# Performance work log

Hardware: AMD Instinct MI355X
Metric: run time of the kernel (lower is better)

## Reference

```python
import jax, jax.numpy as jnp
import numpy as np

DIM = 1024
EPS = 1e-5


def setup_inputs() -> dict:
    key = jax.random.key(0)
    ks = jax.random.split(key, 7)
    C = DIM
    x = jax.random.normal(ks[0], (4, 4096, C), dtype=jnp.float32)
    norm_w = jnp.ones((C,), dtype=jnp.float32)
    norm_b = jnp.zeros((C,), dtype=jnp.float32)
    s = 1.0 / np.sqrt(C)
    qkv_w = jax.random.uniform(ks[1], (3 * C, C), dtype=jnp.float32, minval=-s, maxval=s)
    qkv_b = jax.random.uniform(ks[2], (3 * C,), dtype=jnp.float32, minval=-s, maxval=s)
    proj_w = jax.random.uniform(ks[3], (C, C), dtype=jnp.float32, minval=-s, maxval=s)
    proj_b = jax.random.uniform(ks[4], (C,), dtype=jnp.float32, minval=-s, maxval=s)
    return {"x": x, "norm_w": norm_w, "norm_b": norm_b, "qkv_w": qkv_w,
            "qkv_b": qkv_b, "proj_w": proj_w, "proj_b": proj_b}


def _layernorm(x, w, b):
    mu = jnp.mean(x, axis=-1, keepdims=True)
    var = jnp.mean(jnp.square(x - mu), axis=-1, keepdims=True)
    return (x - mu) * jax.lax.rsqrt(var + EPS) * w + b


def reference(x, norm_w, norm_b, qkv_w, qkv_b, proj_w, proj_b):
    B, T, C = x.shape
    residual = x
    h = _layernorm(x, norm_w, norm_b)
    qkv = jnp.einsum('btc,oc->bto', h, qkv_w) + qkv_b  # [B,T,3C]
    q, k, v = qkv[..., :C], qkv[..., C:2 * C], qkv[..., 2 * C:]
    attn = jnp.einsum('btc,bsc->bts', q, k) / jnp.sqrt(jnp.float32(C))  # raw QK^T, no softmax
    o = jnp.einsum('bts,bsc->btc', attn, v)
    o = jnp.einsum('btc,oc->bto', o, proj_w) + proj_b
    return residual + o  # dropout is identity in eval mode
```

## Files before the change

kernel.cpp:

```cpp
#include <hip/hip_runtime.h>

typedef _Float16 f16;
typedef _Float16 f16x4 __attribute__((ext_vector_type(4)));
typedef _Float16 f16x8 __attribute__((ext_vector_type(8)));
typedef float f32x4 __attribute__((ext_vector_type(4)));

#define AS1 __attribute__((address_space(1)))
#define AS3 __attribute__((address_space(3)))

__device__ __forceinline__ void gl_lds16(const f16* g, f16* l) {
  __builtin_amdgcn_global_load_lds((const AS1 void*)g, (AS3 void*)l, 16, 0, 0);
}

__global__ __launch_bounds__(256) void ln_kernel(const float* __restrict__ x,
                                                 const float* __restrict__ gw,
                                                 const float* __restrict__ gb,
                                                 f16* __restrict__ H) {
  const int wv = threadIdx.x >> 6, lane = threadIdx.x & 63;
  const long row = (long)blockIdx.x * 4 + wv;
  const float* xr = x + row * 1024;
  float4 v[4];
  float s = 0.f, s2 = 0.f;
#pragma unroll
  for (int j = 0; j < 4; ++j) {
    v[j] = ((const float4*)xr)[lane + 64 * j];
    s  += v[j].x + v[j].y + v[j].z + v[j].w;
    s2 += v[j].x * v[j].x + v[j].y * v[j].y + v[j].z * v[j].z + v[j].w * v[j].w;
  }
#pragma unroll
  for (int off = 32; off > 0; off >>= 1) {
    s  += __shfl_xor(s, off);
    s2 += __shfl_xor(s2, off);
  }
  const float mu = s * (1.0f / 1024.0f);
  const float rstd = rsqrtf(s2 * (1.0f / 1024.0f) - mu * mu + 1e-5f);
#pragma unroll
  for (int j = 0; j < 4; ++j) {
    const float4 w4 = ((const float4*)gw)[lane + 64 * j];
    const float4 b4 = ((const float4*)gb)[lane + 64 * j];
    f16x4 h;
    h[0] = (f16)((v[j].x - mu) * rstd * w4.x + b4.x);
    h[1] = (f16)((v[j].y - mu) * rstd * w4.y + b4.y);
    h[2] = (f16)((v[j].z - mu) * rstd * w4.z + b4.z);
    h[3] = (f16)((v[j].w - mu) * rstd * w4.w + b4.w);
    *(f16x4*)(H + row * 1024 + (lane + 64 * j) * 4) = h;
  }
}

__global__ __launch_bounds__(256) void transpose_cs_kernel(const f16* __restrict__ H,
                                                           f16* __restrict__ Ht,
                                                           float* __restrict__ hs) {
  __shared__ f16 tile[64][68];
  __shared__ float csum[4][64];
  const int b = blockIdx.z;
  const long Hb  = (long)b * 4096 * 1024;
  const long Htb = (long)b * 1024 * 4096;
  const int t0 = blockIdx.y * 64, c0 = blockIdx.x * 64;
  const int tid = threadIdx.x;
  const int r = tid >> 2, g0 = tid & 3;
#pragma unroll
  for (int i = 0; i < 4; ++i) {
    const int g = g0 + i * 4;
    f16x4 v = *(const f16x4*)(H + Hb + (long)(t0 + r) * 1024 + c0 + g * 4);
    *(f16x4*)&tile[r][g * 4] = v;
  }
  __syncthreads();
  {
    const int cl = tid & 63, rg = tid >> 6;
    float s = 0.f;
#pragma unroll
    for (int rr = 0; rr < 16; ++rr) s += (float)tile[rg * 16 + rr][cl];
    csum[rg][cl] = s;
  }
#pragma unroll
  for (int i = 0; i < 4; ++i) {
    const int g = g0 + i * 4;
    f16x4 v;
    v[0] = tile[g * 4 + 0][r];
    v[1] = tile[g * 4 + 1][r];
    v[2] = tile[g * 4 + 2][r];
    v[3] = tile[g * 4 + 3][r];
    *(f16x4*)(Ht + Htb + (long)(c0 + r) * 4096 + t0 + g * 4) = v;
  }
  __syncthreads();
  if (tid < 64)
    atomicAdd(&hs[b * 1024 + c0 + tid],
              csum[0][tid] + csum[1][tid] + csum[2][tid] + csum[3][tid]);
}

__global__ __launch_bounds__(256) void transcast4(const float* __restrict__ qkv_w,
                                                  const float* __restrict__ proj_w,
                                                  f16* __restrict__ WT3,
                                                  f16* __restrict__ Wh,
                                                  f16* __restrict__ Ph) {
  const int z = blockIdx.z;
  __shared__ f16 tile[64][68];
  const int r0 = blockIdx.y * 64, c0 = blockIdx.x * 64;
  const int tid = threadIdx.x;
  const int r = tid >> 2, g0 = tid & 3;
  if (z == 3) {
#pragma unroll
    for (int i = 0; i < 4; ++i) {
      const int g = g0 + i * 4;
      float4 v = *(const float4*)(proj_w + (long)(r0 + r) * 1024 + c0 + g * 4);
      f16x4 h; h[0]=(f16)v.x; h[1]=(f16)v.y; h[2]=(f16)v.z; h[3]=(f16)v.w;
      *(f16x4*)(Ph + (long)(r0 + r) * 1024 + c0 + g * 4) = h;
    }
    return;
  }
  const float* W = qkv_w + (long)z * 1048576;
  f16* WT = WT3 + (long)z * 1048576;
#pragma unroll
  for (int i = 0; i < 4; ++i) {
    const int g = g0 + i * 4;
    float4 v = *(const float4*)(W + (long)(r0 + r) * 1024 + c0 + g * 4);
    f16x4 h; h[0]=(f16)v.x; h[1]=(f16)v.y; h[2]=(f16)v.z; h[3]=(f16)v.w;
    *(f16x4*)&tile[r][g * 4] = h;
    if (z >= 1)
      *(f16x4*)(Wh + (long)z * 1048576 + (long)(r0 + r) * 1024 + c0 + g * 4) = h;
  }
  __syncthreads();
#pragma unroll
  for (int i = 0; i < 4; ++i) {
    const int g = g0 + i * 4;
    f16x4 v;
    v[0] = tile[g * 4 + 0][r];
    v[1] = tile[g * 4 + 1][r];
    v[2] = tile[g * 4 + 2][r];
    v[3] = tile[g * 4 + 3][r];
    *(f16x4*)(WT + (long)(c0 + r) * 1024 + r0 + g * 4) = v;
  }
}

__device__ __forceinline__ float dot1024(const f16* __restrict__ row,
                                         const float* __restrict__ v) {
  const int lane = threadIdx.x & 63;
  float s = 0.f;
#pragma unroll
  for (int j = 0; j < 2; ++j) {
    const int d = (lane + 64 * j) * 8;
    f16x8 a = *(const f16x8*)(row + d);
    float4 h0 = *(const float4*)(v + d);
    float4 h1 = *(const float4*)(v + d + 4);
    s += (float)a[0] * h0.x + (float)a[1] * h0.y + (float)a[2] * h0.z + (float)a[3] * h0.w
       + (float)a[4] * h1.x + (float)a[5] * h1.y + (float)a[6] * h1.z + (float)a[7] * h1.w;
  }
#pragma unroll
  for (int off = 32; off > 0; off >>= 1) s += __shfl_down(s, off);
  return s;
}

__device__ __forceinline__ float dotf1024(const float* __restrict__ a,
                                          const float* __restrict__ v) {
  const int lane = threadIdx.x & 63;
  float s = 0.f;
#pragma unroll
  for (int j = 0; j < 4; ++j) {
    const int d = (lane + 64 * j) * 4;
    float4 x = *(const float4*)(a + d);
    float4 q = *(const float4*)(v + d);
    s += x.x * q.x + x.y * q.y + x.z * q.z + x.w * q.w;
  }
#pragma unroll
  for (int off = 32; off > 0; off >>= 1) s += __shfl_down(s, off);
  return s;
}

__global__ void gemv3a(const f16* __restrict__ WT3, const f16* __restrict__ Ph,
                       const float* __restrict__ qkv_b, float* __restrict__ ayd,
                       float* __restrict__ scal) {
  if (blockIdx.x == 3072) {
    float s = dotf1024(qkv_b + 1024, qkv_b);
    if ((threadIdx.x & 63) == 0) scal[4] = s;
    return;
  }
  const int which = blockIdx.x >> 10, m = blockIdx.x & 1023;
  const f16* row;
  const float* v;
  if (which == 0)      { row = WT3 + (long)m * 1024;            v = qkv_b + 1024; }
  else if (which == 1) { row = WT3 + 1048576 + (long)m * 1024;  v = qkv_b; }
  else                 { row = Ph + (long)m * 1024;             v = qkv_b + 2048; }
  float s = dot1024(row, v);
  if ((threadIdx.x & 63) == 0) ayd[which * 1024 + m] = s;
}

__global__ void gemv3b(const f16* __restrict__ U, const f16* __restrict__ PWv,
                       const f16* __restrict__ Gh, const float* __restrict__ hs,
                       const float* __restrict__ ayd, float* __restrict__ efz,
                       float* __restrict__ scal) {
  if (blockIdx.x >= 12288) {
    const int b = blockIdx.x - 12288;
    float s = dotf1024(hs + b * 1024, ayd + 1024);
    if ((threadIdx.x & 63) == 0) scal[b] = s;
    return;
  }
  const int sel = blockIdx.x >> 12, r = blockIdx.x & 4095;
  const int b = r >> 10, m = r & 1023;
  const f16* row;
  const float* v;
  if (sel == 0)      { row = U + (long)m * 1024;                       v = hs + b * 1024; }
  else if (sel == 1) { row = PWv + (long)m * 1024;                     v = hs + b * 1024; }
  else               { row = Gh + (long)b * 1048576 + (long)m * 1024;  v = ayd + 1024; }
  float s = dot1024(row, v);
  if ((threadIdx.x & 63) == 0) efz[sel * 4096 + r] = s;
}

__global__ void gemvC2n(const f16* __restrict__ PWv, const float* __restrict__ efz,
                        const float* __restrict__ ayd, const float* __restrict__ scal,
                        const float* __restrict__ proj_b, float* __restrict__ c2) {
  const int b = blockIdx.x >> 10, c = blockIdx.x & 1023;
  float s = dot1024(PWv + (long)c * 1024, efz + 8192 + b * 1024);
  if ((threadIdx.x & 63) == 0) {
    const float d = ayd[2048 + c];
    c2[b * 1024 + c] = (s + d * scal[b] + scal[4] * (efz[4096 + b * 1024 + c] + 4096.f * d))
                         * 0.03125f + proj_b[c];
  }
}

#define GP64_COMMON()                                        \
  const int tid = threadIdx.x;                               \
  const int wave = tid >> 6, lane = tid & 63;                \
  const int lr = lane & 15, lk = lane >> 4;                  \
  const int srow = tid >> 3;                                 \
  const int slc  = (tid & 7) ^ (srow & 7);                   \
  const int kc0 = ((lk) ^ (lr & 7)) * 8;                     \
  const int kc1 = ((4 + lk) ^ (lr & 7)) * 8;

#define GEMM_WAIT8(NBUF_, r_)                                               \
  do {                                                                      \
    if constexpr (NBUF_ == 3) {                                             \
      if ((r_) >= 2)      asm volatile("s_waitcnt vmcnt(16)" ::: "memory"); \
      else if ((r_) == 1) asm volatile("s_waitcnt vmcnt(8)" ::: "memory");  \
      else                asm volatile("s_waitcnt vmcnt(0)" ::: "memory");  \
    } else {                                                                \
      if ((r_) >= 1)      asm volatile("s_waitcnt vmcnt(8)" ::: "memory");  \
      else                asm volatile("s_waitcnt vmcnt(0)" ::: "memory");  \
    }                                                                       \
  } while (0)

#define COMP64_HALF(asb_, bsb_, kc_)                                             \
  do {                                                                           \
    const f16* asb = (asb_);                                                     \
    const f16* bsb = (bsb_);                                                     \
    f16x8 af[4], bf[4];                                                          \
    _Pragma("unroll")                                                            \
    for (int mi = 0; mi < 4; ++mi)                                               \
      af[mi] = *(const f16x8*)(asb + (wm * 64 + mi * 16 + lr) * 64 + (kc_));     \
    _Pragma("unroll")                                                            \
    for (int ni = 0; ni < 4; ++ni)                                               \
      bf[ni] = *(const f16x8*)(bsb + (wn * 64 + ni * 16 + lr) * 64 + (kc_));     \
    _Pragma("unroll")                                                            \
    for (int mi = 0; mi < 4; ++mi)                                               \
      _Pragma("unroll")                                                          \
      for (int ni = 0; ni < 4; ++ni)                                             \
        acc[mi][ni] = __builtin_amdgcn_mfma_f32_16x16x32_f16(af[mi], bf[ni],     \
                                                             acc[mi][ni], 0, 0, 0); \
  } while (0)

#define GEMM_BODY_LOOP(NBUF_, NT_, STAGEM)                       \
  do {                                                           \
    if constexpr (NBUF_ == 3) {                                  \
      STAGEM(0, 0); STAGEM(1, 1);                                \
      int cur = 0, stg = 2;                                      \
      for (int t = 0; t < (NT_); ++t) {                          \
        if (t + 2 < (NT_)) STAGEM(stg, t + 2);                   \
        GEMM_WAIT8(3, (NT_) - 1 - t);                            \
        asm volatile("s_barrier" ::: "memory");                  \
        __builtin_amdgcn_s_setprio(1);                           \
        COMP64_HALF(&As[cur][0], &Bs[cur][0], kc0);              \
        COMP64_HALF(&As[cur][0], &Bs[cur][0], kc1);              \
        __builtin_amdgcn_s_setprio(0);                           \
        asm volatile("s_waitcnt lgkmcnt(0)" ::: "memory");       \
        asm volatile("s_barrier" ::: "memory");                  \
        cur = (cur + 1 == 3) ? 0 : cur + 1;                      \
        stg = (stg + 1 == 3) ? 0 : stg + 1;                      \
      }                                                          \
    } else {                                                     \
      STAGEM(0, 0);                                              \
      int cur = 0;                                               \
      for (int t = 0; t < (NT_); ++t) {                          \
        if (t + 1 < (NT_)) STAGEM(cur ^ 1, t + 1);               \
        GEMM_WAIT8(2, (NT_) - 1 - t);                            \
        asm volatile("s_barrier" ::: "memory");                  \
        __builtin_amdgcn_s_setprio(1);                           \
        COMP64_HALF(&As[cur][0], &Bs[cur][0], kc0);              \
        COMP64_HALF(&As[cur][0], &Bs[cur][0], kc1);              \
        __builtin_amdgcn_s_setprio(0);                           \
        asm volatile("s_waitcnt lgkmcnt(0)" ::: "memory");       \
        asm volatile("s_barrier" ::: "memory");                  \
        cur ^= 1;                                                \
      }                                                          \
    }                                                            \
  } while (0)

template <int MODE>
__global__ __launch_bounds__(256) void gemm128(
    const f16* __restrict__ A, const f16* __restrict__ B, int K,
    long sA, long sB, long sC,
    f16* __restrict__ Ch,
    const float* __restrict__ dvec, const float* __restrict__ evec,
    const float* __restrict__ fvec, const float* __restrict__ avec) {
  const int b = blockIdx.z;
  A += (long)b * sA;
  B += (long)b * sB;
  const int nx = blockIdx.y & 7;
  const int ny = blockIdx.x;

  GP64_COMMON();
  const int wm = wave >> 1, wn = wave & 1;

  __shared__ __align__(16) f16 As[3][8192];
  __shared__ __align__(16) f16 Bs[3][8192];

  const long aoffs = (long)(ny * 128 + srow) * K + slc * 8;
  const long boffs = (long)(nx * 128 + srow) * K + slc * 8;

  f32x4 zero = {0.f, 0.f, 0.f, 0.f};
  f32x4 acc[4][4];
#pragma unroll
  for (int mi = 0; mi < 4; ++mi)
#pragma unroll
    for (int ni = 0; ni < 4; ++ni) acc[mi][ni] = zero;

#define STAGE(buf, kt)                                                              \
  do {                                                                              \
    f16* asb = &As[buf][0];                                                         \
    f16* bsb = &Bs[buf][0];                                                         \
    _Pragma("unroll")                                                               \
    for (int q = 0; q < 4; ++q) {                                                   \
      gl_lds16(A + aoffs + (long)q * 32 * K + (kt) * 64, asb + q * 2048 + tid * 8); \
      gl_lds16(B + boffs + (long)q * 32 * K + (kt) * 64, bsb + q * 2048 + tid * 8); \
    }                                                                               \
  } while (0)

  const int nt = K >> 6;
  GEMM_BODY_LOOP(3, nt, STAGE);
#undef STAGE

  const long cb = (long)b * sC;
  const int m0 = ny * 128 + wm * 64;
  const int n0 = nx * 128 + wn * 64;
#pragma unroll
  for (int mi = 0; mi < 4; ++mi)
#pragma unroll
    for (int ni = 0; ni < 4; ++ni)
#pragma unroll
      for (int j = 0; j < 4; ++j) {
        const int gm = m0 + mi * 16 + lk * 4 + j;
        const int gn = n0 + ni * 16 + lr;
        float val = acc[mi][ni][j];
        if constexpr (MODE == 0) {
          Ch[cb + (long)gm * 1024 + gn] = (f16)val;
        } else {
          const float dm = dvec[gm];
          const float fm = fvec[b * 1024 + gm];
          const float en = evec[b * 1024 + gn];
          const float an = avec[gn];
          val = (val + dm * en + (fm + 4096.f * dm) * an) * 0.03125f;
          Ch[cb + (long)gm * 1024 + gn] = (f16)val;
        }
      }
}

__global__ __launch_bounds__(256) void gemmGUV(const f16* __restrict__ Ht,
                                               const f16* __restrict__ WT3,
                                               const f16* __restrict__ Ph,
                                               f16* __restrict__ part,
                                               f16* __restrict__ U,
                                               f16* __restrict__ PWv) {
  GP64_COMMON();
  const int wm = wave >> 1, wn = wave & 1;

  __shared__ __align__(16) f16 As[2][8192];
  __shared__ __align__(16) f16 Bs[2][8192];

  const int bid = blockIdx.x;
  const f16 *Ab, *Bb;
  long rs;
  int tileid = 0, zz = 0, selt = 0;
  if (bid < 576) {
    zz = bid & 15;
    tileid = bid >> 4;
    const int b = zz & 3, ks4 = zz >> 2;
    int ti = 0, trem = tileid;
    while (trem >= 8 - ti) { trem -= 8 - ti; ++ti; }
    const int tj = ti + trem;
    const f16* Hb = Ht + (long)b * 4194304;
    rs = 4096;
    Ab = Hb + (long)(ti * 128 + srow) * 4096 + (long)ks4 * 1024 + slc * 8;
    Bb = Hb + (long)(tj * 128 + srow) * 4096 + (long)ks4 * 1024 + slc * 8;
  } else {
    const int u = bid - 576;
    selt = (u >> 6) + 1;
    const int t = u & 63;
    const int ny = t >> 3, nxx = t & 7;
    const f16* A0 = (selt == 2) ? Ph : WT3;
    const f16* B0 = (selt == 2) ? (WT3 + 2097152) : (WT3 + 1048576);
    rs = 1024;
    Ab = A0 + (long)(ny * 128 + srow) * 1024 + slc * 8;
    Bb = B0 + (long)(nxx * 128 + srow) * 1024 + slc * 8;
  }

  f32x4 zero = {0.f, 0.f, 0.f, 0.f};
  f32x4 acc[4][4];
#pragma unroll
  for (int mi = 0; mi < 4; ++mi)
#pragma unroll
    for (int ni = 0; ni < 4; ++ni) acc[mi][ni] = zero;

#define SAq(buf, kt, q) gl_lds16(Ab + (long)(q) * 32 * rs + (kt) * 64, &As[buf][(q) * 2048] + tid * 8)
#define SBq(buf, kt, q) gl_lds16(Bb + (long)(q) * 32 * rs + (kt) * 64, &Bs[buf][(q) * 2048] + tid * 8)

  const int nt = 16;
  SBq(0, 0, 0); SBq(0, 0, 1); SBq(0, 0, 2); SBq(0, 0, 3);
  SAq(0, 0, 0); SAq(0, 0, 2); SAq(0, 0, 1); SAq(0, 0, 3);

  int cur = 0;
  for (int t = 0; t < nt; ++t) {
    const f16* asb = &As[cur][0];
    const f16* bsb = &Bs[cur][0];
    const int nb = cur ^ 1;
    const bool st = (t + 1 < nt);
    f16x8 bf[4][2], af[2][2];

    asm volatile("s_waitcnt vmcnt(2)" ::: "memory");
    asm volatile("s_barrier" ::: "memory");
#pragma unroll
    for (int ni = 0; ni < 4; ++ni) {
      bf[ni][0] = *(const f16x8*)(bsb + (wn * 64 + ni * 16 + lr) * 64 + kc0);
      bf[ni][1] = *(const f16x8*)(bsb + (wn * 64 + ni * 16 + lr) * 64 + kc1);
    }
#pragma unroll
    for (int mi = 0; mi < 2; ++mi) {
      af[mi][0] = *(const f16x8*)(asb + (wm * 64 + mi * 16 + lr) * 64 + kc0);
      af[mi][1] = *(const f16x8*)(asb + (wm * 64 + mi * 16 + lr) * 64 + kc1);
    }
    if (st) { SBq(nb, t + 1, 0); SBq(nb, t + 1, 1); SBq(nb, t + 1, 2); SBq(nb, t + 1, 3);
              SAq(nb, t + 1, 0); SAq(nb, t + 1, 2); }
    asm volatile("s_waitcnt lgkmcnt(0)" ::: "memory");
    __builtin_amdgcn_s_setprio(1);
#pragma unroll
    for (int ks = 0; ks < 2; ++ks)
#pragma unroll
      for (int mi = 0; mi < 2; ++mi)
#pragma unroll
        for (int ni = 0; ni < 4; ++ni)
          acc[mi][ni] = __builtin_amdgcn_mfma_f32_16x16x32_f16(af[mi][ks], bf[ni][ks],
                                                               acc[mi][ni], 0, 0, 0);
    __builtin_amdgcn_s_setprio(0);
    asm volatile("s_barrier" ::: "memory");

    if (st) asm volatile("s_waitcnt vmcnt(6)" ::: "memory");
    else    asm volatile("s_waitcnt vmcnt(0)" ::: "memory");
    asm volatile("s_barrier" ::: "memory");
#pragma unroll
    for (int mi = 0; mi < 2; ++mi) {
      af[mi][0] = *(const f16x8*)(asb + (wm * 64 + (mi + 2) * 16 + lr) * 64 + kc0);
      af[mi][1] = *(const f16x8*)(asb + (wm * 64 + (mi + 2) * 16 + lr) * 64 + kc1);
    }
    if (st) { SAq(nb, t + 1, 1); SAq(nb, t + 1, 3); }
    asm volatile("s_waitcnt lgkmcnt(0)" ::: "memory");
    __builtin_amdgcn_s_setprio(1);
#pragma unroll
    for (int ks = 0; ks < 2; ++ks)
#pragma unroll
      for (int mi = 0; mi < 2; ++mi)
#pragma unroll
        for (int ni = 0; ni < 4; ++ni)
          acc[mi + 2][ni] = __builtin_amdgcn_mfma_f32_16x16x32_f16(af[mi][ks], bf[ni][ks],
                                                                   acc[mi + 2][ni], 0, 0, 0);
    __builtin_amdgcn_s_setprio(0);
    asm volatile("s_barrier" ::: "memory");

    cur ^= 1;
  }
#undef SAq
#undef SBq

  if (selt == 0) {
    f16* P = part + ((long)zz * 36 + tileid) * 16384;
#pragma unroll
    for (int mi = 0; mi < 4; ++mi)
#pragma unroll
      for (int ni = 0; ni < 4; ++ni)
#pragma unroll
        for (int j = 0; j < 4; ++j) {
          const int gm = wm * 64 + mi * 16 + lk * 4 + j;
          const int gn = wn * 64 + ni * 16 + lr;
          P[gm * 128 + gn] = (f16)acc[mi][ni][j];
        }
  } else {
    const int u = bid - 576;
    const int t = u & 63;
    const int ny = t >> 3, nxx = t & 7;
    f16* C = (selt == 2) ? PWv : U;
    const int m0 = ny * 128 + wm * 64;
    const int n0 = nxx * 128 + wn * 64;
#pragma unroll
    for (int mi = 0; mi < 4; ++mi)
#pragma unroll
      for (int ni = 0; ni < 4; ++ni)
#pragma unroll
        for (int j = 0; j < 4; ++j) {
          const int gm = m0 + mi * 16 + lk * 4 + j;
          const int gn = n0 + ni * 16 + lr;
          C[(long)gm * 1024 + gn] = (f16)acc[mi][ni][j];
        }
  }
}

__global__ __launch_bounds__(512) void gemm256f(
    const f16* __restrict__ A,
    const f16* __restrict__ Bw,
    const float* __restrict__ resid,
    const float* __restrict__ c2v,
    float* __restrict__ outF) {
  const int lin = blockIdx.y * 4 + blockIdx.x;
  const int xcd = lin & 7, slot = lin >> 3;
  const int ny = xcd * 8 + (slot >> 2);
  const int nx = slot & 3;
  const int bb = ny >> 4;

  GP64_COMMON();
  const int wm = wave >> 2, wn = wave & 3;

  __shared__ __align__(16) f16 As[2][16384];
  __shared__ __align__(16) f16 Bs[2][16384];

  const f16* Ab = A + (long)ny * 262144;
  const f16* Bb = Bw + (long)bb * 1048576 + (long)nx * 262144;
  const long offs = (long)srow * 1024 + slc * 8;

  f32x4 zero = {0.f, 0.f, 0.f, 0.f};
  f32x4 acc[8][4];
#pragma unroll
  for (int mi = 0; mi < 8; ++mi)
#pragma unroll
    for (int ni = 0; ni < 4; ++ni) acc[mi][ni] = zero;

#define SA(buf, kt, q) gl_lds16(Ab + offs + (long)(q) * 65536 + (kt) * 64, &As[buf][(q) * 4096] + tid * 8)
#define SB(buf, kt, q) gl_lds16(Bb + offs + (long)(q) * 65536 + (kt) * 64, &Bs[buf][(q) * 4096] + tid * 8)

#define RD_BF(dst, bsb, kc)                                                       \
  _Pragma("unroll")                                                               \
  for (int ni = 0; ni < 4; ++ni)                                                  \
    dst[ni] = *(const f16x8*)((bsb) + (wn * 64 + ni * 16 + lr) * 64 + (kc));
#define RD_AF(dst, asb, mh, kc)                                                   \
  _Pragma("unroll")                                                               \
  for (int mi = 0; mi < 4; ++mi)                                                  \
    dst[mi] = *(const f16x8*)((asb) + (wm * 128 + (mh) * 64 + mi * 16 + lr) * 64 + (kc));
#define MF16(af_, bf_, mo)                                                        \
  __builtin_amdgcn_s_setprio(1);                                                  \
  _Pragma("unroll")                                                               \
  for (int mi = 0; mi < 4; ++mi)                                                  \
    _Pragma("unroll")                                                             \
    for (int ni = 0; ni < 4; ++ni)                                                \
      acc[(mo) + mi][ni] = __builtin_amdgcn_mfma_f32_16x16x32_f16(af_[mi], bf_[ni], \
                                                                  acc[(mo) + mi][ni], 0, 0, 0); \
  __builtin_amdgcn_s_setprio(0);

  const int nt = 16;
  SB(0, 0, 0); SB(0, 0, 1); SB(0, 0, 2); SB(0, 0, 3);
  SA(0, 0, 0); SA(0, 0, 2); SA(0, 0, 1); SA(0, 0, 3);

  int cur = 0;
  for (int t = 0; t < nt; ++t) {
    const f16* asb = &As[cur][0];
    const f16* bsb = &Bs[cur][0];
    const int nb = cur ^ 1;
    const bool st = (t + 1 < nt);
    f16x8 bf[4], af[4];

    asm volatile("s_waitcnt vmcnt(2)" ::: "memory");
    asm volatile("s_barrier" ::: "memory");
    RD_BF(bf, bsb, kc0);
    RD_AF(af, asb, 0, kc0);
    if (st) { SB(nb, t + 1, 0); SB(nb, t + 1, 1); }
    asm volatile("s_waitcnt lgkmcnt(0)" ::: "memory");
    MF16(af, bf, 0);
    asm volatile("s_barrier" ::: "memory");

    if (st) asm volatile("s_waitcnt vmcnt(2)" ::: "memory");
    else    asm volatile("s_waitcnt vmcnt(0)" ::: "memory");
    asm volatile("s_barrier" ::: "memory");
    RD_AF(af, asb, 1, kc0);
    if (st) { SB(nb, t + 1, 2); SB(nb, t + 1, 3); }
    asm volatile("s_waitcnt lgkmcnt(0)" ::: "memory");
    MF16(af, bf, 4);
    asm volatile("s_barrier" ::: "memory");

    RD_BF(bf, bsb, kc1);
    RD_AF(af, asb, 0, kc1);
    if (st) { SA(nb, t + 1, 0); SA(nb, t + 1, 2); }
    asm volatile("s_waitcnt lgkmcnt(0)" ::: "memory");
    MF16(af, bf, 0);
    asm volatile("s_barrier" ::: "memory");

    RD_AF(af, asb, 1, kc1);
    if (st) { SA(nb, t + 1, 1); SA(nb, t + 1, 3); }
    asm volatile("s_waitcnt lgkmcnt(0)" ::: "memory");
    MF16(af, bf, 4);
    asm volatile("s_barrier" ::: "memory");

    cur ^= 1;
  }
#undef SA
#undef SB
#undef RD_BF
#undef RD_AF
#undef MF16

  asm volatile("s_waitcnt vmcnt(0)" ::: "memory");
  asm volatile("s_barrier" ::: "memory");

  float* weps = ((float*)&As[0][0]) + wave * 1088;
  const int m0 = ny * 256 + wm * 128;
  const int n0 = nx * 256 + wn * 64;
  const int err = lane >> 3;
  const int ecc = (lane & 7) * 4;
  float4 cc2[2];
#pragma unroll
  for (int q = 0; q < 2; ++q)
    cc2[q] = *(const float4*)&c2v[bb * 1024 + n0 + ecc + 32 * q];

#pragma unroll
  for (int mi = 0; mi < 8; ++mi) {
#pragma unroll
    for (int ni = 0; ni < 4; ++ni)
#pragma unroll
      for (int j = 0; j < 4; ++j)
        weps[(lk * 4 + j) * 68 + ni * 16 + lr] = acc[mi][ni][j];
    asm volatile("s_waitcnt lgkmcnt(0)" ::: "memory");
#pragma unroll
    for (int h = 0; h < 2; ++h)
#pragma unroll
      for (int q = 0; q < 2; ++q) {
        const int rr = err + 8 * h;
        const int cc = ecc + 32 * q;
        float4 o = *(const float4*)&weps[rr * 68 + cc];
        const long gbase = (long)(m0 + mi * 16 + rr) * 1024 + n0 + cc;
        const float4 rv = *(const float4*)&resid[gbase];
        float4 ov;
        ov.x = o.x + rv.x + cc2[q].x;
        ov.y = o.y + rv.y + cc2[q].y;
        ov.z = o.z + rv.z + cc2[q].z;
        ov.w = o.w + rv.w + cc2[q].w;
        *(float4*)&outF[gbase] = ov;
      }
  }
}

__global__ __launch_bounds__(256) void treduce(const f16* __restrict__ part,
                                               f16* __restrict__ Gh) {
  const int tileid = blockIdx.x, b = blockIdx.y;
  int ti = 0, trem = tileid;
  while (trem >= 8 - ti) { trem -= 8 - ti; ++ti; }
  const int tj = ti + trem;
  __shared__ f16 tl[128][132];
  const int tid = threadIdx.x;
  f16* Gb = Gh + (long)b * 1048576;
#pragma unroll
  for (int it = 0; it < 16; ++it) {
    const int e = it * 1024 + tid * 4;
    const int r = e >> 7, c = e & 127;
    f16x4 p0 = *(const f16x4*)(part + ((long)(0 * 4 + b) * 36 + tileid) * 16384 + e);
    f16x4 p1 = *(const f16x4*)(part + ((long)(1 * 4 + b) * 36 + tileid) * 16384 + e);
    f16x4 p2 = *(const f16x4*)(part + ((long)(2 * 4 + b) * 36 + tileid) * 16384 + e);
    f16x4 p3 = *(const f16x4*)(part + ((long)(3 * 4 + b) * 36 + tileid) * 16384 + e);
    f16x4 sv;
#pragma unroll
    for (int j = 0; j < 4; ++j)
      sv[j] = (f16)((float)p0[j] + (float)p1[j] + (float)p2[j] + (float)p3[j]);
    *(f16x4*)(Gb + (long)(ti * 128 + r) * 1024 + tj * 128 + c) = sv;
    *(f16x4*)&tl[r][c] = sv;
  }
  if (ti != tj) {
    __syncthreads();
#pragma unroll
    for (int it = 0; it < 16; ++it) {
      const int e = it * 1024 + tid * 4;
      const int r = e >> 7, c = e & 127;
      f16x4 v;
      v[0] = tl[c + 0][r];
      v[1] = tl[c + 1][r];
      v[2] = tl[c + 2][r];
      v[3] = tl[c + 3][r];
      *(f16x4*)(Gb + (long)(tj * 128 + r) * 1024 + ti * 128 + c) = v;
    }
  }
}

extern "C" void kernel_launch(void* const* d_in, const int* in_sizes, int n_in,
                              void* d_out, int out_size, void* d_ws, size_t ws_size,
                              hipStream_t stream) {
  const float* x      = (const float*)d_in[0];
  const float* norm_w = (const float*)d_in[1];
  const float* norm_b = (const float*)d_in[2];
  const float* qkv_w  = (const float*)d_in[3];
  const float* qkv_b  = (const float*)d_in[4];
  const float* proj_w = (const float*)d_in[5];
  const float* proj_b = (const float*)d_in[6];
  float* out = (float*)d_out;
  char* ws = (char*)d_ws;

  const size_t OFF_H    = 0;
  const size_t OFF_HT   = 33554432;
  const size_t OFF_T1   = 33554432;
  const size_t OFF_T2   = 41943040;
  const size_t OFF_WH   = 67108864;
  const size_t OFF_PH   = 73400320;
  const size_t OFF_WT3  = 75497472;
  const size_t OFF_U    = 81788928;
  const size_t OFF_PWV  = 83886080;
  const size_t OFF_GH   = 85983232;
  const size_t OFF_PART = 94371840;
  const size_t OFF_HS   = 115343360;
  const size_t OFF_AYD  = 115392512;
  const size_t OFF_SCAL = 115404800;
  const size_t OFF_EFZ  = 115405824;
  const size_t OFF_C2   = 115471360;

  f16* H    = (f16*)(ws + OFF_H);
  f16* Ht   = (f16*)(ws + OFF_HT);
  f16* T1   = (f16*)(ws + OFF_T1);
  f16* T2   = (f16*)(ws + OFF_T2);
  f16* Wh   = (f16*)(ws + OFF_WH);
  f16* Ph   = (f16*)(ws + OFF_PH);
  f16* WT3  = (f16*)(ws + OFF_WT3);
  f16* U    = (f16*)(ws + OFF_U);
  f16* PWv  = (f16*)(ws + OFF_PWV);
  f16* Gh   = (f16*)(ws + OFF_GH);
  f16* part = (f16*)(ws + OFF_PART);
  float* hs   = (float*)(ws + OFF_HS);
  float* ayd  = (float*)(ws + OFF_AYD);
  float* scal = (float*)(ws + OFF_SCAL);
  float* efz  = (float*)(ws + OFF_EFZ);
  float* c2v  = (float*)(ws + OFF_C2);

  transcast4<<<dim3(16, 16, 4), 256, 0, stream>>>(qkv_w, proj_w, WT3, Wh, Ph);
  gemv3a<<<dim3(3073), 64, 0, stream>>>(WT3, Ph, qkv_b, ayd, scal);

  ln_kernel<<<dim3(4096), 256, 0, stream>>>(x, norm_w, norm_b, H);
  hipMemsetAsync(ws + OFF_HS, 0, 16384, stream);
  transpose_cs_kernel<<<dim3(16, 64, 4), 256, 0, stream>>>(H, Ht, hs);

  gemmGUV<<<dim3(704), 256, 0, stream>>>(Ht, WT3, Ph, part, U, PWv);
  treduce<<<dim3(36, 4), 256, 0, stream>>>(part, Gh);

  gemv3b<<<dim3(12292), 64, 0, stream>>>(U, PWv, Gh, hs, ayd, efz, scal);
  gemvC2n<<<dim3(4096), 64, 0, stream>>>(PWv, efz, ayd, scal, proj_b, c2v);

  gemm128<0><<<dim3(8, 8, 4), 256, 0, stream>>>(U, Gh, 1024, 0L, 1048576L, 1048576L,
      T1, nullptr, nullptr, nullptr, nullptr);
  gemm128<1><<<dim3(8, 8, 4), 256, 0, stream>>>(PWv, T1, 1024, 0L, 1048576L, 1048576L,
      T2, ayd + 2048, efz, efz + 4096, ayd);

  gemm256f<<<dim3(4, 64), 512, 0, stream>>>(H, T2, x, c2v, out);
}
```

Measured before the change: 190.0 us.

## Replace triple-buffered GEMM loop with split-phase double-buffered pipeline

Measured after the change: 185.6 us. 1.02x faster.

```diff
diff --git a/kernel.cpp b/kernel.cpp
--- a/kernel.cpp
+++ b/kernel.cpp
@@ -226,71 +226,12 @@
   const int kc0 = ((lk) ^ (lr & 7)) * 8;                     \
   const int kc1 = ((4 + lk) ^ (lr & 7)) * 8;
 
-#define GEMM_WAIT8(NBUF_, r_)                                               \
-  do {                                                                      \
-    if constexpr (NBUF_ == 3) {                                             \
-      if ((r_) >= 2)      asm volatile("s_waitcnt vmcnt(16)" ::: "memory"); \
-      else if ((r_) == 1) asm volatile("s_waitcnt vmcnt(8)" ::: "memory");  \
-      else                asm volatile("s_waitcnt vmcnt(0)" ::: "memory");  \
-    } else {                                                                \
-      if ((r_) >= 1)      asm volatile("s_waitcnt vmcnt(8)" ::: "memory");  \
-      else                asm volatile("s_waitcnt vmcnt(0)" ::: "memory");  \
-    }                                                                       \
-  } while (0)
-
-#define COMP64_HALF(asb_, bsb_, kc_)                                             \
-  do {                                                                           \
-    const f16* asb = (asb_);                                                     \
-    const f16* bsb = (bsb_);                                                     \
-    f16x8 af[4], bf[4];                                                          \
-    _Pragma("unroll")                                                            \
-    for (int mi = 0; mi < 4; ++mi)                                               \
-      af[mi] = *(const f16x8*)(asb + (wm * 64 + mi * 16 + lr) * 64 + (kc_));     \
-    _Pragma("unroll")                                                            \
-    for (int ni = 0; ni < 4; ++ni)                                               \
-      bf[ni] = *(const f16x8*)(bsb + (wn * 64 + ni * 16 + lr) * 64 + (kc_));     \
-    _Pragma("unroll")                                                            \
-    for (int mi = 0; mi < 4; ++mi)                                               \
-      _Pragma("unroll")                                                          \
-      for (int ni = 0; ni < 4; ++ni)                                             \
-        acc[mi][ni] = __builtin_amdgcn_mfma_f32_16x16x32_f16(af[mi], bf[ni],     \
-                                                             acc[mi][ni], 0, 0, 0); \
-  } while (0)
-
-#define GEMM_BODY_LOOP(NBUF_, NT_, STAGEM)                       \
-  do {                                                           \
-    if constexpr (NBUF_ == 3) {                                  \
-      STAGEM(0, 0); STAGEM(1, 1);                                \
-      int cur = 0, stg = 2;                                      \
-      for (int t = 0; t < (NT_); ++t) {                          \
-        if (t + 2 < (NT_)) STAGEM(stg, t + 2);                   \
-        GEMM_WAIT8(3, (NT_) - 1 - t);                            \
-        asm volatile("s_barrier" ::: "memory");                  \
-        __builtin_amdgcn_s_setprio(1);                           \
-        COMP64_HALF(&As[cur][0], &Bs[cur][0], kc0);              \
-        COMP64_HALF(&As[cur][0], &Bs[cur][0], kc1);              \
-        __builtin_amdgcn_s_setprio(0);                           \
-        asm volatile("s_waitcnt lgkmcnt(0)" ::: "memory");       \
-        asm volatile("s_barrier" ::: "memory");                  \
-        cur = (cur + 1 == 3) ? 0 : cur + 1;                      \
-        stg = (stg + 1 == 3) ? 0 : stg + 1;                      \
-      }                                                          \
-    } else {                                                     \
-      STAGEM(0, 0);                                              \
-      int cur = 0;                                               \
-      for (int t = 0; t < (NT_); ++t) {                          \
-        if (t + 1 < (NT_)) STAGEM(cur ^ 1, t + 1);               \
-        GEMM_WAIT8(2, (NT_) - 1 - t);                            \
-        asm volatile("s_barrier" ::: "memory");                  \
-        __builtin_amdgcn_s_setprio(1);                           \
-        COMP64_HALF(&As[cur][0], &Bs[cur][0], kc0);              \
-        COMP64_HALF(&As[cur][0], &Bs[cur][0], kc1);              \
-        __builtin_amdgcn_s_setprio(0);                           \
-        asm volatile("s_waitcnt lgkmcnt(0)" ::: "memory");       \
-        asm volatile("s_barrier" ::: "memory");                  \
-        cur ^= 1;                                                \
-      }                                                          \
-    }                                                            \
+#define FINE2_BODY(NT_)                                                           \
+  do {                                                                            \
+    SAq(0, 0, 0); SAq(0, 0, 2);                                                   \
+    int cur = 0;                                                                  \
+                                         \
+    (void)cur;                                                                    \
   } while (0)
 
 template <int MODE>
@@ -309,11 +250,12 @@
   GP64_COMMON();
   const int wm = wave >> 1, wn = wave & 1;
 
-  __shared__ __align__(16) f16 As[3][8192];
-  __shared__ __align__(16) f16 Bs[3][8192];
-
-  const long aoffs = (long)(ny * 128 + srow) * K + slc * 8;
-  const long boffs = (long)(nx * 128 + srow) * K + slc * 8;
+  __shared__ __align__(16) f16 As[2][8192];
+  __shared__ __align__(16) f16 Bs[2][8192];
+
+  const f16* Ab = A + (long)(ny * 128 + srow) * K + slc * 8;
+  const f16* Bb = B + (long)(nx * 128 + srow) * K + slc * 8;
+  const long rs = K;
 
   f32x4 zero = {0.f, 0.f, 0.f, 0.f};
   f32x4 acc[4][4];
@@ -322,20 +264,74 @@
 #pragma unroll
     for (int ni = 0; ni < 4; ++ni) acc[mi][ni] = zero;
 
-#define STAGE(buf, kt)                                                              \
-  do {                                                                              \
-    f16* asb = &As[buf][0];                                                         \
-    f16* bsb = &Bs[buf][0];                                                         \
-    _Pragma("unroll")                                                               \
-    for (int q = 0; q < 4; ++q) {                                                   \
-      gl_lds16(A + aoffs + (long)q * 32 * K + (kt) * 64, asb + q * 2048 + tid * 8); \
-      gl_lds16(B + boffs + (long)q * 32 * K + (kt) * 64, bsb + q * 2048 + tid * 8); \
-    }                                                                               \
-  } while (0)
+#define SAq(buf, kt, q) gl_lds16(Ab + (long)(q) * 32 * rs + (kt) * 64, &As[buf][(q) * 2048] + tid * 8)
+#define SBq(buf, kt, q) gl_lds16(Bb + (long)(q) * 32 * rs + (kt) * 64, &Bs[buf][(q) * 2048] + tid * 8)
 
   const int nt = K >> 6;
-  GEMM_BODY_LOOP(3, nt, STAGE);
-#undef STAGE
+  SBq(0, 0, 0); SBq(0, 0, 1); SBq(0, 0, 2); SBq(0, 0, 3);
+  SAq(0, 0, 0); SAq(0, 0, 2); SAq(0, 0, 1); SAq(0, 0, 3);
+
+  int cur = 0;
+  for (int t = 0; t < nt; ++t) {
+    const f16* asb = &As[cur][0];
+    const f16* bsb = &Bs[cur][0];
+    const int nb = cur ^ 1;
+    const bool st = (t + 1 < nt);
+    f16x8 bf[4][2], af[2][2];
+
+    asm volatile("s_waitcnt vmcnt(2)" ::: "memory");
+    asm volatile("s_barrier" ::: "memory");
+#pragma unroll
+    for (int ni = 0; ni < 4; ++ni) {
+      bf[ni][0] = *(const f16x8*)(bsb + (wn * 64 + ni * 16 + lr) * 64 + kc0);
+      bf[ni][1] = *(const f16x8*)(bsb + (wn * 64 + ni * 16 + lr) * 64 + kc1);
+    }
+#pragma unroll
+    for (int mi = 0; mi < 2; ++mi) {
+      af[mi][0] = *(const f16x8*)(asb + (wm * 64 + mi * 16 + lr) * 64 + kc0);
+      af[mi][1] = *(const f16x8*)(asb + (wm * 64 + mi * 16 + lr) * 64 + kc1);
+    }
+    if (st) { SBq(nb, t + 1, 0); SBq(nb, t + 1, 1); SBq(nb, t + 1, 2); SBq(nb, t + 1, 3);
+              SAq(nb, t + 1, 0); SAq(nb, t + 1, 2); }
+    asm volatile("s_waitcnt lgkmcnt(0)" ::: "memory");
+    __builtin_amdgcn_s_setprio(1);
+#pragma unroll
+    for (int ks = 0; ks < 2; ++ks)
+#pragma unroll
+      for (int mi = 0; mi < 2; ++mi)
+#pragma unroll
+        for (int ni = 0; ni < 4; ++ni)
+          acc[mi][ni] = __builtin_amdgcn_mfma_f32_16x16x32_f16(af[mi][ks], bf[ni][ks],
+                                                               acc[mi][ni], 0, 0, 0);
+    __builtin_amdgcn_s_setprio(0);
+    asm volatile("s_barrier" ::: "memory");
+
+    if (st) asm volatile("s_waitcnt vmcnt(6)" ::: "memory");
+    else    asm volatile("s_waitcnt vmcnt(0)" ::: "memory");
+    asm volatile("s_barrier" ::: "memory");
+#pragma unroll
+    for (int mi = 0; mi < 2; ++mi) {
+      af[mi][0] = *(const f16x8*)(asb + (wm * 64 + (mi + 2) * 16 + lr) * 64 + kc0);
+      af[mi][1] = *(const f16x8*)(asb + (wm * 64 + (mi + 2) * 16 + lr) * 64 + kc1);
+    }
+    if (st) { SAq(nb, t + 1, 1); SAq(nb, t + 1, 3); }
+    asm volatile("s_waitcnt lgkmcnt(0)" ::: "memory");
+    __builtin_amdgcn_s_setprio(1);
+#pragma unroll
+    for (int ks = 0; ks < 2; ++ks)
+#pragma unroll
+      for (int mi = 0; mi < 2; ++mi)
+#pragma unroll
+        for (int ni = 0; ni < 4; ++ni)
+          acc[mi + 2][ni] = __builtin_amdgcn_mfma_f32_16x16x32_f16(af[mi][ks], bf[ni][ks],
+                                                                   acc[mi + 2][ni], 0, 0, 0);
+    __builtin_amdgcn_s_setprio(0);
+    asm volatile("s_barrier" ::: "memory");
+
+    cur ^= 1;
+  }
+#undef SAq
+#undef SBq
 
   const long cb = (long)b * sC;
   const int m0 = ny * 128 + wm * 64;
```
